# Performance work log

Measured on AMD Instinct MI355X. Metric: run time of the kernel, lower is better.

Reference implementation:

```python
import math
import jax, jax.numpy as jnp
import numpy as np

B, S, IN_DIM = 4, 2048, 256
L, H, NHEAD, FFN = 3, 256, 4, 1024
CF, CB = 32, 32  # context_forward / context_backward window
EPS = 1e-5


def sinusoidal_pe(seq_len, d_model):
    pos = jnp.arange(seq_len, dtype=jnp.float32)[:, None]
    div = jnp.exp(jnp.arange(0, d_model, 2, dtype=jnp.float32) * (-math.log(10000.0) / d_model))
    pe = jnp.zeros((seq_len, d_model), dtype=jnp.float32)
    pe = pe.at[:, 0::2].set(jnp.sin(pos * div))
    pe = pe.at[:, 1::2].set(jnp.cos(pos * div))
    return pe


def band_mask(s):
    # True = allowed: -CB <= j - i <= CF (sliding window, from triu/transpose construction)
    i = jnp.arange(s)[:, None]
    j = jnp.arange(s)[None, :]
    return (j - i <= CF) & (i - j <= CB)


def layer_norm(x, g, b):
    mu = jnp.mean(x, axis=-1, keepdims=True)
    var = jnp.mean((x - mu) ** 2, axis=-1, keepdims=True)
    return (x - mu) * jax.lax.rsqrt(var + EPS) * g + b


def mha(x, wqkv, bqkv, wo, bo, mask):
    b, s, d = x.shape
    dh = d // NHEAD
    qkv = x @ wqkv.T + bqkv  # [b, s, 3d]
    q, k, v = jnp.split(qkv, 3, axis=-1)
    split = lambda t: t.reshape(b, s, NHEAD, dh).transpose(0, 2, 1, 3)  # [b, h, s, dh]
    q, k, v = split(q), split(k), split(v)
    scores = jnp.einsum('bhqd,bhkd->bhqk', q, k) / math.sqrt(dh)
    scores = jnp.where(mask, scores, -jnp.inf)
    attn = jax.nn.softmax(scores, axis=-1)
    o = jnp.einsum('bhqk,bhkd->bhqd', attn, v).transpose(0, 2, 1, 3).reshape(b, s, d)
    return o @ wo.T + bo


def setup_inputs() -> dict:
    key = jax.random.key(0)
    ks = jax.random.split(key, 12)
    sc = 0.02
    inp = {
        'x': jax.random.normal(ks[0], (B, S, IN_DIM), dtype=jnp.float32),
        'w_in': sc * jax.random.normal(ks[1], (H, IN_DIM), dtype=jnp.float32),
        'w_out': sc * jax.random.normal(ks[2], (IN_DIM, H), dtype=jnp.float32),
        'b_out': jnp.zeros((IN_DIM,), dtype=jnp.float32),
        'qkv_w': sc * jax.random.normal(ks[3], (L, 3 * H, H), dtype=jnp.float32),
        'qkv_b': jnp.zeros((L, 3 * H), dtype=jnp.float32),
        'out_w': sc * jax.random.normal(ks[4], (L, H, H), dtype=jnp.float32),
        'out_b': jnp.zeros((L, H), dtype=jnp.float32),
        'ln1_g': jnp.ones((L, H), dtype=jnp.float32),
        'ln1_b': jnp.zeros((L, H), dtype=jnp.float32),
        'ln2_g': jnp.ones((L, H), dtype=jnp.float32),
        'ln2_b': jnp.zeros((L, H), dtype=jnp.float32),
        'ff1_w': sc * jax.random.normal(ks[5], (L, FFN, H), dtype=jnp.float32),
        'ff1_b': jnp.zeros((L, FFN), dtype=jnp.float32),
        'ff2_w': sc * jax.random.normal(ks[6], (L, H, FFN), dtype=jnp.float32),
        'ff2_b': jnp.zeros((L, H), dtype=jnp.float32),
        'lnf_g': jnp.ones((H,), dtype=jnp.float32),
        'lnf_b': jnp.zeros((H,), dtype=jnp.float32),
    }
    return inp


def reference(x, w_in, w_out, b_out, qkv_w, qkv_b, out_w, out_b,
              ln1_g, ln1_b, ln2_g, ln2_b, ff1_w, ff1_b, ff2_w, ff2_b,
              lnf_g, lnf_b):
    b, s, _ = x.shape
    mask = band_mask(s)
    h = math.sqrt(H) * (x @ w_in.T) + sinusoidal_pe(s, H)[None]
    for l in range(L):  # pre-norm transformer encoder layers (relu FFN, eval/no-dropout)
        h = h + mha(layer_norm(h, ln1_g[l], ln1_b[l]), qkv_w[l], qkv_b[l], out_w[l], out_b[l], mask)
        z = layer_norm(h, ln2_g[l], ln2_b[l])
        h = h + (jax.nn.relu(z @ ff1_w[l].T + ff1_b[l]) @ ff2_w[l].T + ff2_b[l])
    h = layer_norm(h, lnf_g, lnf_b)
    return h @ w_out.T + b_out
```

## Files before the change

kernel.cpp:

```cpp
#include <hip/hip_runtime.h>
#include <hip/hip_bf16.h>
#include <math.h>

#define SEQ 2048
#define BATCH 4
#define HDIM 256
#define NHEAD 4
#define FFN_DIM 1024
#define MTOT (BATCH*SEQ)

typedef __attribute__((ext_vector_type(8))) short bf16x8;
typedef __attribute__((ext_vector_type(4))) float f32x4;

__device__ __forceinline__ bf16x8 cvt8(const float* p)
{
    float4 a = *(const float4*)p;
    float4 b = *(const float4*)(p + 4);
    union { bf16x8 v; __hip_bfloat16 e[8]; } u;
    u.e[0] = __float2bfloat16(a.x); u.e[1] = __float2bfloat16(a.y);
    u.e[2] = __float2bfloat16(a.z); u.e[3] = __float2bfloat16(a.w);
    u.e[4] = __float2bfloat16(b.x); u.e[5] = __float2bfloat16(b.y);
    u.e[6] = __float2bfloat16(b.z); u.e[7] = __float2bfloat16(b.w);
    return u.v;
}

__global__ __launch_bounds__(256)
void cvt_all(const float* __restrict__ w_in, const float* __restrict__ w_out,
             const float* __restrict__ qkv_w, const float* __restrict__ out_w,
             const float* __restrict__ ff1_w, const float* __restrict__ ff2_w,
             __hip_bfloat16* __restrict__ wb)
{
    int i = blockIdx.x * 256 + threadIdx.x;
    size_t e = (size_t)i * 8;

    const float* srcbase; size_t rbase; int kshift;
    if (e < 720896) {
        if (e < 65536)       { srcbase = w_in;  rbase = 0;      kshift = 8; }
        else if (e < 131072) { srcbase = w_out; rbase = 65536;  kshift = 8; }
        else                 { srcbase = qkv_w; rbase = 131072; kshift = 8; }
    } else if (e < 917504)   { srcbase = out_w; rbase = 720896; kshift = 8; }
    else if (e < 1703936)    { srcbase = ff1_w; rbase = 917504; kshift = 8; }
    else                     { srcbase = ff2_w; rbase = 1703936; kshift = 10; }

    size_t local = e - rbase;
    int K = 1 << kshift;
    int row = (int)(local >> kshift);
    int k   = (int)(local & (K - 1));

    size_t dst = rbase
               + ((size_t)(row >> 4) * (K >> 5) + (k >> 5)) * 512
               + (size_t)((((k >> 3) & 3) << 4) | (row & 15)) * 8;

    *(bf16x8*)(wb + dst) = cvt8(srcbase + local);
}

__device__ __forceinline__ bf16x8 fragW(const short* W, int n0, int k0, int K, int lane)
{
    return *(const bf16x8*)(W + ((size_t)(n0 >> 4) * (K >> 5) + (k0 >> 5)) * 512 + lane * 8);
}

__global__ __launch_bounds__(256)
void embed_pe(const float* __restrict__ X, const __hip_bfloat16* __restrict__ W,
              float* __restrict__ hbuf)
{
    int tid = threadIdx.x, wave = tid >> 6, lane = tid & 63;
    int wm = wave >> 1, wn = wave & 1;
    int rowBase = blockIdx.y * 64 + wm * 32;
    int colBase = blockIdx.x * 64 + wn * 32;
    int lr = lane & 15, hi = lane >> 4;

    const float* px0 = X + (size_t)(rowBase + lr) * HDIM + hi * 8;
    const float* px1 = px0 + (size_t)16 * HDIM;
    const short* Wb  = (const short*)W;

    f32x4 acc[2][2];
    acc[0][0] = (f32x4){0.f,0.f,0.f,0.f}; acc[0][1] = (f32x4){0.f,0.f,0.f,0.f};
    acc[1][0] = (f32x4){0.f,0.f,0.f,0.f}; acc[1][1] = (f32x4){0.f,0.f,0.f,0.f};

    #pragma unroll
    for (int k0 = 0; k0 < 256; k0 += 32) {
        bf16x8 a0 = cvt8(px0 + k0);
        bf16x8 a1 = cvt8(px1 + k0);
        bf16x8 b0 = fragW(Wb, colBase,      k0, 256, lane);
        bf16x8 b1 = fragW(Wb, colBase + 16, k0, 256, lane);
        acc[0][0] = __builtin_amdgcn_mfma_f32_16x16x32_bf16(a0, b0, acc[0][0], 0,0,0);
        acc[0][1] = __builtin_amdgcn_mfma_f32_16x16x32_bf16(a0, b1, acc[0][1], 0,0,0);
        acc[1][0] = __builtin_amdgcn_mfma_f32_16x16x32_bf16(a1, b0, acc[1][0], 0,0,0);
        acc[1][1] = __builtin_amdgcn_mfma_f32_16x16x32_bf16(a1, b1, acc[1][1], 0,0,0);
    }

    int cc = lane & 15, quad = lane >> 4;
    #pragma unroll
    for (int mt = 0; mt < 2; mt++)
        #pragma unroll
        for (int nt = 0; nt < 2; nt++) {
            int col = colBase + nt*16 + cc;
            int i2 = col & ~1;
            float freq = __expf((float)i2 * (-9.210340371976184f / 256.0f));
            #pragma unroll
            for (int r = 0; r < 4; r++) {
                int row = rowBase + mt*16 + quad*4 + r;
                float arg = (float)(row & (SEQ-1)) * freq;
                float pe = (col & 1) ? __cosf(arg) : __sinf(arg);
                hbuf[(size_t)row*HDIM + col] = 16.0f*acc[mt][nt][r] + pe;
            }
        }
}

template<int MODE, int NT>
__global__ __launch_bounds__(256)
void gemm_ln(const float* __restrict__ h,
             const float* __restrict__ g, const float* __restrict__ bln,
             const __hip_bfloat16* __restrict__ W,
             const float* __restrict__ bias,
             __hip_bfloat16* __restrict__ obf, float* __restrict__ of32,
             int N, int ldw)
{
    constexpr int NTW = NT / 32;
    __shared__ __align__(16) short A_lds[64][264];

    int tid = threadIdx.x, wave = tid >> 6, lane = tid & 63;
    int wm = wave >> 1, wn = wave & 1;
    int rowBase = blockIdx.y * 64;
    int colBase = blockIdx.x * NT + wn * (NT / 2);

    {
        float4 gv = *(const float4*)(g + lane * 4);
        float4 bv = *(const float4*)(bln + lane * 4);
        #pragma unroll
        for (int rr = 0; rr < 16; rr += 4) {
            float4 xv[4];
            #pragma unroll
            for (int u = 0; u < 4; u++)
                xv[u] = *(const float4*)(h + (size_t)(rowBase + wave*16 + rr + u)*HDIM + lane*4);
            #pragma unroll
            for (int u = 0; u < 4; u++) {
                float s = xv[u].x + xv[u].y + xv[u].z + xv[u].w;
                #pragma unroll
                for (int off = 32; off >= 1; off >>= 1) s += __shfl_xor(s, off);
                float mu = s * (1.0f/256.0f);
                float d0 = xv[u].x-mu, d1 = xv[u].y-mu, d2 = xv[u].z-mu, d3 = xv[u].w-mu;
                float v = d0*d0 + d1*d1 + d2*d2 + d3*d3;
                #pragma unroll
                for (int off = 32; off >= 1; off >>= 1) v += __shfl_xor(v, off);
                float rstd = rsqrtf(v * (1.0f/256.0f) + 1e-5f);
                union { short e[4]; uint2 w2; } o;
                o.e[0] = (short)__bfloat16_as_ushort(__float2bfloat16(d0*rstd*gv.x + bv.x));
                o.e[1] = (short)__bfloat16_as_ushort(__float2bfloat16(d1*rstd*gv.y + bv.y));
                o.e[2] = (short)__bfloat16_as_ushort(__float2bfloat16(d2*rstd*gv.z + bv.z));
                o.e[3] = (short)__bfloat16_as_ushort(__float2bfloat16(d3*rstd*gv.w + bv.w));
                *(uint2*)&A_lds[wave*16 + rr + u][lane*4] = o.w2;
            }
        }
    }
    __syncthreads();

    int lr = lane & 15, hi = lane >> 4;
    f32x4 acc[2][NTW];
    #pragma unroll
    for (int mt = 0; mt < 2; mt++)
        #pragma unroll
        for (int nt = 0; nt < NTW; nt++)
            acc[mt][nt] = (f32x4){0.f,0.f,0.f,0.f};

    const short* Ws = (const short*)W;
    #pragma unroll
    for (int k0 = 0; k0 < 256; k0 += 32) {
        bf16x8 af[2], bfr[NTW];
        #pragma unroll
        for (int mt = 0; mt < 2; mt++)
            af[mt] = *(const bf16x8*)&A_lds[wm*32 + mt*16 + lr][k0 + hi*8];
        #pragma unroll
        for (int nt = 0; nt < NTW; nt++)
            bfr[nt] = fragW(Ws, colBase + nt*16, k0, 256, lane);
        #pragma unroll
        for (int mt = 0; mt < 2; mt++)
            #pragma unroll
            for (int nt = 0; nt < NTW; nt++)
                acc[mt][nt] = __builtin_amdgcn_mfma_f32_16x16x32_bf16(af[mt], bfr[nt], acc[mt][nt], 0,0,0);
    }

    int cc = lane & 15, quad = lane >> 4;
    #pragma unroll
    for (int mt = 0; mt < 2; mt++)
        #pragma unroll
        for (int nt = 0; nt < NTW; nt++) {
            int col = colBase + nt*16 + cc;
            float bv = bias[col];
            #pragma unroll
            for (int r = 0; r < 4; r++) {
                int row = rowBase + wm*32 + mt*16 + quad*4 + r;
                float c = acc[mt][nt][r] + bv;
                if (MODE == 4) { of32[(size_t)row*N + col] = c; }
                else {
                    int sec = col >> 8, hd = (col >> 6) & 3, d = col & 63;
                    int srow = row & (SEQ - 1);
                    size_t base = (size_t)sec * 2097152
                                + (size_t)(((row >> 11) << 2) | hd) * 131072;
                    size_t idx;
                    if (sec < 2)
                        idx = base + (size_t)(srow >> 4) * 1024 + (size_t)(d >> 5) * 512
                            + (size_t)((((d >> 3) & 3) << 4) | (srow & 15)) * 8 + (d & 7);
                    else
                        idx = base + (size_t)srow * 64 + d;
                    obf[idx] = __float2bfloat16(c);
                }
            }
        }
}

struct AttnLDS {
    __align__(16) __hip_bfloat16 Vt[64][128];
    __align__(16) __hip_bfloat16 Pl[32][96];
    float sm[2][32], ss[2][32];
};

__global__ __launch_bounds__(1024)
void attn_ffn(const __hip_bfloat16* __restrict__ qkvd,
              const __hip_bfloat16* __restrict__ ow,
              const float* __restrict__ ob,
              float* __restrict__ h,
              const float* __restrict__ g, const float* __restrict__ bln,
              const __hip_bfloat16* __restrict__ W1, const float* __restrict__ b1,
              const __hip_bfloat16* __restrict__ W2, const float* __restrict__ b2)
{
    __shared__ union SMem {
        AttnLDS asl[4];
        struct {
            __align__(16) short A[32][264];
            __align__(16) short Z[2][32][264];
        } f;
    } U;
    __shared__ __align__(16) short att_lds[32][264];
    __shared__ __align__(16) float H_lds[32][260];

    int tid  = threadIdx.x;
    int wave = tid >> 6, lane = tid & 63;
    int grp  = wave >> 2, w4 = wave & 3, ltid = tid & 255;
    int b    = blockIdx.y, i0 = blockIdx.x * 32;
    int klo  = i0 - 32;

    int lr = lane & 15, hi = lane >> 4;
    int cc = lane & 15, quad = lane >> 4;

    int hd = grp;
    AttnLDS& S = U.asl[grp];
    const short* Qd = (const short*)qkvd + (size_t)(b * 4 + hd) * 131072;
    const short* Kd = Qd + 2097152;
    const short* Vd = Qd + 4194304;
    int qh = w4 & 1, seg = w4 >> 1;
    int qoff = qh * 16 + quad * 4;

    int vm = ltid & 7, vrl = ltid >> 3, vdp = vm * 8;
    bf16x8 vr[3];
    #pragma unroll
    for (int rr = 0; rr < 3; rr++) {
        int j = klo + rr * 32 + vrl;
        j = j < 0 ? 0 : (j > SEQ - 1 ? SEQ - 1 : j);
        vr[rr] = *(const bf16x8*)(Vd + (size_t)j * 64 + vdp);
    }
    bf16x8 qf[2];
    #pragma unroll
    for (int ds = 0; ds < 2; ds++)
        qf[ds] = *(const bf16x8*)(Qd + (size_t)((i0 >> 4) + qh) * 1024 + ds * 512 + lane * 8);
    bf16x8 kf[3][2];
    #pragma unroll
    for (int t = 0; t < 3; t++) {
        int jt = (klo + seg * 48 + t * 16) >> 4;
        jt = jt < 0 ? 0 : (jt > 127 ? 127 : jt);
        kf[t][0] = *(const bf16x8*)(Kd + (size_t)jt * 1024 + lane * 8);
        kf[t][1] = *(const bf16x8*)(Kd + (size_t)jt * 1024 + 512 + lane * 8);
    }
    float hold[2][4];
    {
        const float* hp = h + (size_t)(b * SEQ + i0) * HDIM + wave * 16 + cc;
        #pragma unroll
        for (int mt = 0; mt < 2; mt++)
            #pragma unroll
            for (int r = 0; r < 4; r++)
                hold[mt][r] = hp[(size_t)(mt*16 + quad*4 + r) * HDIM];
    }

    {
        union { bf16x8 v; short e[8]; } u;
        #pragma unroll
        for (int rr = 0; rr < 3; rr++) {
            int row = rr * 32 + vrl;
            int colp = row ^ (vm << 3);
            u.v = vr[rr];
            #pragma unroll
            for (int jj = 0; jj < 8; jj++)
                *(short*)&S.Vt[vdp + jj][colp] = u.e[jj];
        }
    }

    f32x4 sacc[3];
    #pragma unroll
    for (int t = 0; t < 3; t++) {
        f32x4 a = (f32x4){0.f,0.f,0.f,0.f};
        a = __builtin_amdgcn_mfma_f32_16x16x32_bf16(qf[0], kf[t][0], a, 0,0,0);
        a = __builtin_amdgcn_mfma_f32_16x16x32_bf16(qf[1], kf[t][1], a, 0,0,0);
        sacc[t] = a;
    }

    float s[3][4];
    #pragma unroll
    for (int t = 0; t < 3; t++) {
        int koff = seg * 48 + t * 16 + cc;
        int jj = klo + koff;
        #pragma unroll
        for (int r = 0; r < 4; r++) {
            int rel = koff - (qoff + r);
            bool ok = (jj >= 0) && (jj < SEQ) && (rel >= 0) && (rel <= 64);
            s[t][r] = ok ? sacc[t][r] * 0.125f : -1e30f;
        }
    }

    float mrow[4], srow[4];
    #pragma unroll
    for (int r = 0; r < 4; r++)
        mrow[r] = fmaxf(fmaxf(s[0][r], s[1][r]), s[2][r]);
    #pragma unroll
    for (int off = 8; off >= 1; off >>= 1)
        #pragma unroll
        for (int r = 0; r < 4; r++)
            mrow[r] = fmaxf(mrow[r], __shfl_xor(mrow[r], off));
    #pragma unroll
    for (int r = 0; r < 4; r++)
        srow[r] = __expf(s[0][r]-mrow[r]) + __expf(s[1][r]-mrow[r]) + __expf(s[2][r]-mrow[r]);
    #pragma unroll
    for (int off = 8; off >= 1; off >>= 1)
        #pragma unroll
        for (int r = 0; r < 4; r++)
            srow[r] += __shfl_xor(srow[r], off);
    if (cc == 0) {
        #pragma unroll
        for (int r = 0; r < 4; r++) { S.sm[seg][qoff+r] = mrow[r]; S.ss[seg][qoff+r] = srow[r]; }
    }
    __syncthreads();

    float Mr[4], inv[4];
    #pragma unroll
    for (int r = 0; r < 4; r++) {
        float m0 = S.sm[0][qoff+r], m1 = S.sm[1][qoff+r];
        float M = fmaxf(m0, m1);
        float dn = S.ss[0][qoff+r] * __expf(m0 - M) + S.ss[1][qoff+r] * __expf(m1 - M);
        Mr[r] = M; inv[r] = 1.0f / dn;
    }
    #pragma unroll
    for (int t = 0; t < 3; t++)
        #pragma unroll
        for (int r = 0; r < 4; r++)
            S.Pl[qoff+r][seg*48 + t*16 + cc] = __float2bfloat16(__expf(s[t][r]-Mr[r]) * inv[r]);
    __syncthreads();

    bf16x8 owf[8];
    {
        const short* op = (const short*)ow + (size_t)wave * 8 * 512 + lane * 8;
        #pragma unroll
        for (int i = 0; i < 8; i++)
            owf[i] = *(const bf16x8*)(op + i * 512);
    }

    {
        f32x4 oacc[2];
        oacc[0] = (f32x4){0.f,0.f,0.f,0.f}; oacc[1] = (f32x4){0.f,0.f,0.f,0.f};
        #pragma unroll
        for (int ks = 0; ks < 3; ks++) {
            int kk = ks * 32;
            bf16x8 pf = *(const bf16x8*)&S.Pl[qh*16 + lr][kk + hi*8];
            #pragma unroll
            for (int dt = 0; dt < 2; dt++) {
                int d = seg*32 + dt*16 + lr;
                int colb = (kk + hi*8) ^ (((d >> 3) & 7) << 3);
                bf16x8 vf = *(const bf16x8*)&S.Vt[d][colb];
                oacc[dt] = __builtin_amdgcn_mfma_f32_16x16x32_bf16(pf, vf, oacc[dt], 0,0,0);
            }
        }
        #pragma unroll
        for (int dt = 0; dt < 2; dt++) {
            int col = hd*64 + seg*32 + dt*16 + cc;
            #pragma unroll
            for (int r = 0; r < 4; r++)
                att_lds[qoff + r][col] =
                    (short)__bfloat16_as_ushort(__float2bfloat16(oacc[dt][r]));
        }
    }
    __syncthreads();

    {
        f32x4 acc[2];
        acc[0] = (f32x4){0.f,0.f,0.f,0.f}; acc[1] = (f32x4){0.f,0.f,0.f,0.f};
        #pragma unroll
        for (int i = 0; i < 8; i++) {
            bf16x8 a0 = *(const bf16x8*)&att_lds[lr][i*32 + hi*8];
            bf16x8 a1 = *(const bf16x8*)&att_lds[16 + lr][i*32 + hi*8];
            acc[0] = __builtin_amdgcn_mfma_f32_16x16x32_bf16(a0, owf[i], acc[0], 0,0,0);
            acc[1] = __builtin_amdgcn_mfma_f32_16x16x32_bf16(a1, owf[i], acc[1], 0,0,0);
        }
        float bv = ob[wave*16 + cc];
        #pragma unroll
        for (int mt = 0; mt < 2; mt++)
            #pragma unroll
            for (int r = 0; r < 4; r++)
                H_lds[mt*16 + quad*4 + r][wave*16 + cc] = hold[mt][r] + acc[mt][r] + bv;
    }

    const short* W1s = (const short*)W1;
    const short* W2s = (const short*)W2;
    bf16x8 w1f[8];
    {
        const short* wp = W1s + (size_t)wave * 8 * 512 + lane * 8;
        #pragma unroll
        for (int i = 0; i < 8; i++)
            w1f[i] = *(const bf16x8*)(wp + i * 512);
    }
    __syncthreads();

    {
        float4 gv = *(const float4*)(g + lane * 4);
        float4 bv = *(const float4*)(bln + lane * 4);
        #pragma unroll
        for (int u = 0; u < 2; u++) {
            float4 xv = *(const float4*)&H_lds[wave*2 + u][lane*4];
            float ss2 = xv.x + xv.y + xv.z + xv.w;
            #pragma unroll
            for (int off = 32; off >= 1; off >>= 1) ss2 += __shfl_xor(ss2, off);
            float mu = ss2 * (1.0f/256.0f);
            float d0 = xv.x-mu, d1 = xv.y-mu, d2 = xv.z-mu, d3 = xv.w-mu;
            float v = d0*d0 + d1*d1 + d2*d2 + d3*d3;
            #pragma unroll
            for (int off = 32; off >= 1; off >>= 1) v += __shfl_xor(v, off);
            float rstd = rsqrtf(v * (1.0f/256.0f) + 1e-5f);
            union { short e[4]; uint2 w2; } o;
            o.e[0] = (short)__bfloat16_as_ushort(__float2bfloat16(d0*rstd*gv.x + bv.x));
            o.e[1] = (short)__bfloat16_as_ushort(__float2bfloat16(d1*rstd*gv.y + bv.y));
            o.e[2] = (short)__bfloat16_as_ushort(__float2bfloat16(d2*rstd*gv.z + bv.z));
            o.e[3] = (short)__bfloat16_as_ushort(__float2bfloat16(d3*rstd*gv.w + bv.w));
            *(uint2*)&U.f.A[wave*2 + u][lane*4] = o.w2;
        }
    }
    __syncthreads();

    f32x4 acc2[2];
    acc2[0] = (f32x4){0.f,0.f,0.f,0.f}; acc2[1] = (f32x4){0.f,0.f,0.f,0.f};

    #pragma unroll 1
    for (int kk = 0; kk < 4; kk++) {
        bf16x8 w2f[8];
        {
            const short* wp = W2s + (size_t)(wave * 32 + kk * 8) * 512 + lane * 8;
            #pragma unroll
            for (int i = 0; i < 8; i++)
                w2f[i] = *(const bf16x8*)(wp + i * 512);
        }

        f32x4 acc1[2];
        acc1[0] = (f32x4){0.f,0.f,0.f,0.f}; acc1[1] = (f32x4){0.f,0.f,0.f,0.f};
        #pragma unroll
        for (int i = 0; i < 8; i++) {
            bf16x8 af0 = *(const bf16x8*)&U.f.A[lr][i*32 + hi*8];
            bf16x8 af1 = *(const bf16x8*)&U.f.A[16 + lr][i*32 + hi*8];
            acc1[0] = __builtin_amdgcn_mfma_f32_16x16x32_bf16(af0, w1f[i], acc1[0], 0,0,0);
            acc1[1] = __builtin_amdgcn_mfma_f32_16x16x32_bf16(af1, w1f[i], acc1[1], 0,0,0);
        }

        {
            int col = wave*16 + cc;
            float bb = b1[kk*256 + col];
            #pragma unroll
            for (int mt = 0; mt < 2; mt++)
                #pragma unroll
                for (int r = 0; r < 4; r++) {
                    float z = fmaxf(acc1[mt][r] + bb, 0.f);
                    U.f.Z[kk & 1][mt*16 + quad*4 + r][col] =
                        (short)__bfloat16_as_ushort(__float2bfloat16(z));
                }
        }
        __syncthreads();

        {
            int nk = (kk < 3) ? kk + 1 : 3;
            const short* wp = W1s + (size_t)(nk * 16 + wave) * 8 * 512 + lane * 8;
            #pragma unroll
            for (int i = 0; i < 8; i++)
                w1f[i] = *(const bf16x8*)(wp + i * 512);
        }

        #pragma unroll
        for (int i = 0; i < 8; i++) {
            bf16x8 zf0 = *(const bf16x8*)&U.f.Z[kk & 1][lr][i*32 + hi*8];
            bf16x8 zf1 = *(const bf16x8*)&U.f.Z[kk & 1][16 + lr][i*32 + hi*8];
            acc2[0] = __builtin_amdgcn_mfma_f32_16x16x32_bf16(zf0, w2f[i], acc2[0], 0,0,0);
            acc2[1] = __builtin_amdgcn_mfma_f32_16x16x32_bf16(zf1, w2f[i], acc2[1], 0,0,0);
        }
    }

    {
        int col = wave*16 + cc;
        float bb = b2[col];
        #pragma unroll
        for (int mt = 0; mt < 2; mt++)
            #pragma unroll
            for (int r = 0; r < 4; r++) {
                int rowl = mt*16 + quad*4 + r;
                int row = b * SEQ + i0 + rowl;
                h[(size_t)row * HDIM + col] = H_lds[rowl][col] + acc2[mt][r] + bb;
            }
    }
}

extern "C" void kernel_launch(void* const* d_in, const int* in_sizes, int n_in,
                              void* d_out, int out_size, void* d_ws, size_t ws_size,
                              hipStream_t stream)
{
    const float* x     = (const float*)d_in[0];
    const float* w_in  = (const float*)d_in[1];
    const float* w_out = (const float*)d_in[2];
    const float* b_out = (const float*)d_in[3];
    const float* qkv_w = (const float*)d_in[4];
    const float* qkv_b = (const float*)d_in[5];
    const float* out_w = (const float*)d_in[6];
    const float* out_b = (const float*)d_in[7];
    const float* ln1_g = (const float*)d_in[8];
    const float* ln1_b = (const float*)d_in[9];
    const float* ln2_g = (const float*)d_in[10];
    const float* ln2_b = (const float*)d_in[11];
    const float* ff1_w = (const float*)d_in[12];
    const float* ff1_b = (const float*)d_in[13];
    const float* ff2_w = (const float*)d_in[14];
    const float* ff2_b = (const float*)d_in[15];
    const float* lnf_g = (const float*)d_in[16];
    const float* lnf_b = (const float*)d_in[17];

    char* ws = (char*)d_ws;
    float*          h    = (float*)ws;
    __hip_bfloat16* qkvd = (__hip_bfloat16*)(ws + 8388608);
    __hip_bfloat16* wb   = (__hip_bfloat16*)(ws + 25165824);

    __hip_bfloat16* w_in_b  = wb;
    __hip_bfloat16* w_out_b = wb + 65536;
    __hip_bfloat16* qkv_w_b = wb + 131072;
    __hip_bfloat16* out_w_b = wb + 720896;
    __hip_bfloat16* ff1_w_b = wb + 917504;
    __hip_bfloat16* ff2_w_b = wb + 1703936;

    dim3 blk(256);

    cvt_all<<<1216, blk, 0, stream>>>(w_in, w_out, qkv_w, out_w, ff1_w, ff2_w, wb);

    embed_pe<<<dim3(4, 128), blk, 0, stream>>>(x, w_in_b, h);

    for (int l = 0; l < 3; l++) {
        gemm_ln<5, 128><<<dim3(6, 128), blk, 0, stream>>>(
            h, ln1_g + l*HDIM, ln1_b + l*HDIM,
            qkv_w_b + (size_t)l*768*HDIM, qkv_b + l*768, qkvd, nullptr, 768, HDIM);
        attn_ffn<<<dim3(SEQ/32, BATCH), dim3(1024), 0, stream>>>(
            qkvd, out_w_b + (size_t)l*HDIM*HDIM, out_b + l*HDIM, h,
            ln2_g + l*HDIM, ln2_b + l*HDIM,
            ff1_w_b + (size_t)l*FFN_DIM*HDIM, ff1_b + l*FFN_DIM,
            ff2_w_b + (size_t)l*HDIM*FFN_DIM, ff2_b + l*HDIM);
    }

    gemm_ln<4, 64><<<dim3(4, 128), blk, 0, stream>>>(
        h, lnf_g, lnf_b, w_out_b, b_out, nullptr, (float*)d_out, HDIM, HDIM);
}
```

Before: 241.8 us.

## Write V in MFMA-fragment layout so attention loads V fragments directly

The QKV GEMM epilogue now stores V pre-tiled in the MFMA B-operand fragment order, so the attention kernel loads V fragments straight from global memory into registers. This drops the LDS transpose of V, its scalar LDS stores and the swizzled LDS reads, and shrinks the per-group LDS footprint. The QKV GEMM tile width also doubles, halving the grid in N. Risks are scattered epilogue stores and fewer blocks for the QKV GEMM.

```diff
diff --git a/kernel.cpp b/kernel.cpp
--- a/kernel.cpp
+++ b/kernel.cpp
@@ -202,7 +202,8 @@
                         idx = base + (size_t)(srow >> 4) * 1024 + (size_t)(d >> 5) * 512
                             + (size_t)((((d >> 3) & 3) << 4) | (srow & 15)) * 8 + (d & 7);
                     else
-                        idx = base + (size_t)srow * 64 + d;
+                        idx = base + ((size_t)(d >> 4) * 64 + (srow >> 5)) * 512
+                            + (size_t)((((srow >> 3) & 3) << 4) | (d & 15)) * 8 + (srow & 7);
                     obf[idx] = __float2bfloat16(c);
                 }
             }
@@ -210,8 +211,7 @@
 }
 
 struct AttnLDS {
-    __align__(16) __hip_bfloat16 Vt[64][128];
-    __align__(16) __hip_bfloat16 Pl[32][96];
+    __align__(16) __hip_bfloat16 Pl[32][104];
     float sm[2][32], ss[2][32];
 };
 
@@ -236,7 +236,7 @@
 
     int tid  = threadIdx.x;
     int wave = tid >> 6, lane = tid & 63;
-    int grp  = wave >> 2, w4 = wave & 3, ltid = tid & 255;
+    int grp  = wave >> 2, w4 = wave & 3;
     int b    = blockIdx.y, i0 = blockIdx.x * 32;
     int klo  = i0 - 32;
 
@@ -251,14 +251,6 @@
     int qh = w4 & 1, seg = w4 >> 1;
     int qoff = qh * 16 + quad * 4;
 
-    int vm = ltid & 7, vrl = ltid >> 3, vdp = vm * 8;
-    bf16x8 vr[3];
-    #pragma unroll
-    for (int rr = 0; rr < 3; rr++) {
-        int j = klo + rr * 32 + vrl;
-        j = j < 0 ? 0 : (j > SEQ - 1 ? SEQ - 1 : j);
-        vr[rr] = *(const bf16x8*)(Vd + (size_t)j * 64 + vdp);
-    }
     bf16x8 qf[2];
     #pragma unroll
     for (int ds = 0; ds < 2; ds++)
@@ -271,6 +263,17 @@
         kf[t][0] = *(const bf16x8*)(Kd + (size_t)jt * 1024 + lane * 8);
         kf[t][1] = *(const bf16x8*)(Kd + (size_t)jt * 1024 + 512 + lane * 8);
     }
+    bf16x8 vf[3][2];
+    #pragma unroll
+    for (int ks = 0; ks < 3; ks++) {
+        int s0 = klo + ks * 32;
+        s0 = s0 < 0 ? 0 : (s0 > SEQ - 32 ? SEQ - 32 : s0);
+        #pragma unroll
+        for (int dt = 0; dt < 2; dt++) {
+            int d0 = seg*32 + dt*16;
+            vf[ks][dt] = *(const bf16x8*)(Vd + ((size_t)(d0 >> 4) * 64 + (s0 >> 5)) * 512 + lane * 8);
+        }
+    }
     float hold[2][4];
     {
         const float* hp = h + (size_t)(b * SEQ + i0) * HDIM + wave * 16 + cc;
@@ -279,19 +282,6 @@
             #pragma unroll
             for (int r = 0; r < 4; r++)
                 hold[mt][r] = hp[(size_t)(mt*16 + quad*4 + r) * HDIM];
-    }
-
-    {
-        union { bf16x8 v; short e[8]; } u;
-        #pragma unroll
-        for (int rr = 0; rr < 3; rr++) {
-            int row = rr * 32 + vrl;
-            int colp = row ^ (vm << 3);
-            u.v = vr[rr];
-            #pragma unroll
-            for (int jj = 0; jj < 8; jj++)
-                *(short*)&S.Vt[vdp + jj][colp] = u.e[jj];
-        }
     }
 
     f32x4 sacc[3];
@@ -367,15 +357,10 @@
         oacc[0] = (f32x4){0.f,0.f,0.f,0.f}; oacc[1] = (f32x4){0.f,0.f,0.f,0.f};
         #pragma unroll
         for (int ks = 0; ks < 3; ks++) {
-            int kk = ks * 32;
-            bf16x8 pf = *(const bf16x8*)&S.Pl[qh*16 + lr][kk + hi*8];
-            #pragma unroll
-            for (int dt = 0; dt < 2; dt++) {
-                int d = seg*32 + dt*16 + lr;
-                int colb = (kk + hi*8) ^ (((d >> 3) & 7) << 3);
-                bf16x8 vf = *(const bf16x8*)&S.Vt[d][colb];
-                oacc[dt] = __builtin_amdgcn_mfma_f32_16x16x32_bf16(pf, vf, oacc[dt], 0,0,0);
-            }
+            bf16x8 pf = *(const bf16x8*)&S.Pl[qh*16 + lr][ks*32 + hi*8];
+            #pragma unroll
+            for (int dt = 0; dt < 2; dt++)
+                oacc[dt] = __builtin_amdgcn_mfma_f32_16x16x32_bf16(pf, vf[ks][dt], oacc[dt], 0,0,0);
         }
         #pragma unroll
         for (int dt = 0; dt < 2; dt++) {
@@ -552,7 +537,7 @@
     embed_pe<<<dim3(4, 128), blk, 0, stream>>>(x, w_in_b, h);
 
     for (int l = 0; l < 3; l++) {
-        gemm_ln<5, 128><<<dim3(6, 128), blk, 0, stream>>>(
+        gemm_ln<5, 256><<<dim3(3, 128), blk, 0, stream>>>(
             h, ln1_g + l*HDIM, ln1_b + l*HDIM,
             qkv_w_b + (size_t)l*768*HDIM, qkv_b + l*768, qkvd, nullptr, 768, HDIM);
         attn_ffn<<<dim3(SEQ/32, BATCH), dim3(1024), 0, stream>>>(
```

After: 259.0 us. 1.07x slower.
